# Kernel tuning notes

Measured on AMD Instinct MI355X. Metric: run time of the kernel, lower is better.

## Reference

```python
import jax, jax.numpy as jnp
import numpy as np

B, D_IN, D_HID, NH, PF = 1024, 2048, 4096, 8, 2
D_UP = D_IN * PF          # 4096
HS = D_HID // NH          # 512 head size
EPS = 1e-5


def setup_inputs() -> dict:
    key = jax.random.key(0)
    ks = jax.random.split(key, 24)
    it = iter(range(24))

    def lin(k, fin, fout):
        # weight stored as (in, out); y = x @ W + b
        return jax.random.normal(k, (fin, fout), jnp.float32) / np.float32(np.sqrt(fin))

    def bd(k, fin_blk, fout_blk):
        # block-diagonal per-head weights (NH, in_blk, out_blk)
        return jax.random.normal(k, (NH, fin_blk, fout_blk), jnp.float32) / np.float32(np.sqrt(fin_blk))

    inp = {}
    inp['x'] = jax.random.normal(ks[next(it)], (B, D_IN), jnp.float32)
    inp['h_prev'] = jax.random.normal(ks[next(it)], (B, D_HID), jnp.float32)
    inp['c_prev'] = jax.random.normal(ks[next(it)], (B, D_HID), jnp.float32)
    inp['n_prev'] = jax.random.normal(ks[next(it)], (B, D_HID), jnp.float32)
    inp['m_prev'] = jax.random.normal(ks[next(it)], (B, D_HID), jnp.float32)
    inp['ln_w'] = jnp.ones((D_IN,), jnp.float32)
    inp['ln_b'] = jnp.zeros((D_IN,), jnp.float32)
    inp['upL_w'] = lin(ks[next(it)], D_IN, D_UP); inp['upL_b'] = jnp.zeros((D_UP,), jnp.float32)
    inp['upR_w'] = lin(ks[next(it)], D_IN, D_HID); inp['upR_b'] = jnp.zeros((D_HID,), jnp.float32)
    inp['conv_w'] = jax.random.normal(ks[next(it)], (1, 1, 4), jnp.float32) * 0.5  # (O,I,K)
    inp['conv_b'] = jnp.zeros((1,), jnp.float32)
    inp['skip_w'] = lin(ks[next(it)], D_UP, D_HID); inp['skip_b'] = jnp.zeros((D_HID,), jnp.float32)
    inp['wq'] = bd(ks[next(it)], D_UP // NH, HS); inp['bq'] = jnp.zeros((NH, HS), jnp.float32)
    inp['wk'] = bd(ks[next(it)], D_UP // NH, HS); inp['bk'] = jnp.zeros((NH, HS), jnp.float32)
    inp['wv'] = bd(ks[next(it)], D_UP // NH, HS); inp['bv'] = jnp.zeros((NH, HS), jnp.float32)
    inp['wi_w'] = lin(ks[next(it)], D_UP, D_HID); inp['wi_b'] = jnp.zeros((D_HID,), jnp.float32)
    inp['wf_w'] = lin(ks[next(it)], D_UP, D_HID); inp['wf_b'] = jnp.zeros((D_HID,), jnp.float32)
    inp['wo_w'] = lin(ks[next(it)], D_UP, D_HID); inp['wo_b'] = jnp.zeros((D_HID,), jnp.float32)
    inp['gn_w'] = jnp.ones((D_HID,), jnp.float32)
    inp['gn_b'] = jnp.zeros((D_HID,), jnp.float32)
    inp['down_w'] = lin(ks[next(it)], D_HID, D_IN); inp['down_b'] = jnp.zeros((D_IN,), jnp.float32)
    return inp


def _forward(x, h_prev, c_prev, n_prev, m_prev, ln_w, ln_b, upL_w, upL_b, upR_w, upR_b,
             conv_w, conv_b, skip_w, skip_b, wq, bq, wk, bk, wv, bv,
             wi_w, wi_b, wf_w, wf_b, wo_w, wo_b, gn_w, gn_b, down_w, down_b):
    b = x.shape[0]
    # LayerNorm(input_size)
    mu = jnp.mean(x, axis=-1, keepdims=True)
    var = jnp.var(x, axis=-1, keepdims=True)
    x_norm = (x - mu) * jax.lax.rsqrt(var + EPS) * ln_w + ln_b

    x_up_left = x_norm @ upL_w + upL_b     # (B, D_UP)
    x_up_right = x_norm @ upR_w + upR_b    # (B, D_HID)

    # CausalConv1D(1,1,4): left-pad 3, valid conv  == torch pad 3 both sides + drop last 3
    conv = jax.lax.conv_general_dilated(
        x_up_left[:, None, :], conv_w, window_strides=(1,), padding=((3, 0),),
        dimension_numbers=('NCH', 'OIH', 'NCH'))
    x_conv = jax.nn.silu(conv[:, 0, :] + conv_b[0])   # (B, D_UP)

    x_skip = x_conv @ skip_w + skip_b                 # (B, D_HID)

    def blockdiag(xv, w, bias):
        xh = xv.reshape(b, NH, -1)                    # (B, NH, in_blk)
        return (jnp.einsum('bhi,hio->bho', xh, w) + bias).reshape(b, -1)

    q = blockdiag(x_conv, wq, bq)                                  # (B, D_HID)
    k = blockdiag(x_conv, wk, bk) / np.float32(np.sqrt(HS))
    v = blockdiag(x_up_left, wv, bv)

    i_tilde = x_conv @ wi_w + wi_b
    f_tilde = x_conv @ wf_w + wf_b
    o = jax.nn.sigmoid(x_up_left @ wo_w + wo_b)

    # stabilized exponential gating
    m_t = jnp.maximum(f_tilde + m_prev, i_tilde)
    i_g = jnp.exp(i_tilde - m_t)
    f_g = jnp.exp(f_tilde + m_prev - m_t)
    c_t = f_g * c_prev + i_g * (v * k)
    n_t = f_g * n_prev + i_g * k

    # torch.max(torch.abs(n_t.T @ q), 1)[0] -> (D_HID,)
    denom = jnp.max(jnp.abs(n_t.T @ q), axis=1)
    h_t = o * (c_t * q) / denom                       # broadcast (B,D_HID)/(D_HID,)

    # GroupNorm(NH, D_HID) on 2D input
    hg = h_t.reshape(b, NH, HS)
    mu_g = jnp.mean(hg, axis=-1, keepdims=True)
    var_g = jnp.var(hg, axis=-1, keepdims=True)
    gn = ((hg - mu_g) * jax.lax.rsqrt(var_g + EPS)).reshape(b, D_HID) * gn_w + gn_b

    out = (gn + x_skip) * jax.nn.silu(x_up_right)
    final = out @ down_w + down_b + x
    return final, h_t, c_t, n_t, m_t


def reference(x, h_prev, c_prev, n_prev, m_prev, ln_w, ln_b, upL_w, upL_b, upR_w, upR_b,
              conv_w, conv_b, skip_w, skip_b, wq, bq, wk, bk, wv, bv,
              wi_w, wi_b, wf_w, wf_b, wo_w, wo_b, gn_w, gn_b, down_w, down_b):
    return _forward(x, h_prev, c_prev, n_prev, m_prev, ln_w, ln_b, upL_w, upL_b, upR_w, upR_b,
                    conv_w, conv_b, skip_w, skip_b, wq, bq, wk, bk, wv, bv,
                    wi_w, wi_b, wf_w, wf_b, wo_w, wo_b, gn_w, gn_b, down_w, down_b)
```

## Files before the change

kernel.cpp:

```cpp
#include <hip/hip_runtime.h>
#include <math.h>

#define B_ROWS 1024
#define D_IN   2048
#define D_HID  4096
#define D_UP   4096
#define NH     8
#define HS     512
#define LN_EPS 1e-5f

typedef __attribute__((ext_vector_type(8))) short bf16x8_t;
typedef __attribute__((ext_vector_type(4))) float f32x4_t;
typedef __attribute__((ext_vector_type(4))) unsigned short us4_t;

__device__ __forceinline__ unsigned short f2bf(float f) {
    unsigned int u = __float_as_uint(f);
    u += 0x7fffu + ((u >> 16) & 1u);
    return (unsigned short)(u >> 16);
}
__device__ __forceinline__ float bf2f(unsigned short u) {
    return __uint_as_float(((unsigned int)u) << 16);
}
__device__ __forceinline__ float sigmoidf_(float x) { return 1.0f / (1.0f + expf(-x)); }
__device__ __forceinline__ float siluf_(float x)    { return x / (1.0f + expf(-x)); }

__device__ __forceinline__ void gload16(const unsigned short* g, unsigned short* l) {
    __builtin_amdgcn_global_load_lds(
        (const __attribute__((address_space(1))) unsigned int*)(const void*)g,
        (__attribute__((address_space(3))) unsigned int*)(void*)l,
        16, 0, 0);
}

#define VMW(n) asm volatile("s_waitcnt vmcnt(" #n ")" ::: "memory")

#define XCD_SWZ()                                                        \
    int bx = blockIdx.x, by = blockIdx.y;                                \
    {                                                                    \
        const int gx_ = gridDim.x;                                       \
        const int n_  = gx_ * gridDim.y;                                 \
        if ((n_ & 7) == 0) {                                             \
            int lin = by * gx_ + bx;                                     \
            const int q8 = n_ >> 3;                                      \
            lin = (lin & 7) * q8 + (lin >> 3);                           \
            bx = lin % gx_; by = lin / gx_;                              \
        }                                                                \
    }

struct MGChunk {
    const unsigned short* A;
    const unsigned short* Bt;
    const float* bias;
    const float* resid;
    float* C;
    unsigned short* C2;
    float* denom;
    float alpha;
    int epi;
};

template<int NCH>
__global__ __launch_bounds__(256, 3) void mg256(
    MGChunk c0, MGChunk c1, MGChunk c2, MGChunk c3,
    int K, int lda, int ldbt, int ldc, int bpc,
    long aB, long wB, long bB, long cB)
{
    const int gx = gridDim.x, gy = gridDim.y;
    const int n = gx * gy;
    const int orig = blockIdx.y * gx + blockIdx.x;
    const int wl = ((n & 7) == 0) ? ((orig & 7) * (n >> 3) + (orig >> 3)) : orig;
    const int bxw = wl / gy;
    const int byw = wl - bxw * gy;
    const int chid = (NCH > 1) ? (bxw / bpc) : 0;
    const int cbx = bxw - chid * bpc;
    const MGChunk ch = (chid == 0) ? c0 : ((chid == 1) ? c1 : ((chid == 2) ? c2 : c3));
    const int bz = blockIdx.z;

    const unsigned short* A  = ch.A  + bz * aB;
    const unsigned short* Bt = ch.Bt + bz * wB;

    __shared__ __align__(16) unsigned short As[2][256][32];
    __shared__ __align__(16) unsigned short Bs[2][128][32];

    const int t = threadIdx.x;
    const int w = t >> 6, l = t & 63;
    const int wrm = w >> 1;
    const int wcn = w & 1;
    const long rowA = (long)byw * 256;
    const long rowB = (long)cbx * 128;

    const int skz = (((l & 3) ^ ((l >> 3) & 3)) << 3);
    const unsigned short* Ag = A  + rowA * (long)lda;
    const unsigned short* Bg = Bt + rowB * (long)ldbt;

    const int lm  = l & 15;
    const int pkz = (((l >> 4) ^ ((l >> 1) & 3)) << 3);

    f32x4_t acc[8][4];
#pragma unroll
    for (int mi = 0; mi < 8; ++mi)
#pragma unroll
        for (int ni = 0; ni < 4; ++ni) acc[mi][ni] = (f32x4_t)0.0f;

#define STAGE(buf, kb)                                                        \
    {                                                                         \
        _Pragma("unroll")                                                     \
        for (int p = 0; p < 4; ++p)                                           \
            gload16(Ag + (long)(w * 64 + p * 16 + (l >> 2)) * lda + (kb) + skz, \
                    &As[buf][w * 64 + p * 16][0]);                            \
        _Pragma("unroll")                                                     \
        for (int p = 0; p < 2; ++p)                                           \
            gload16(Bg + (long)(w * 32 + p * 16 + (l >> 2)) * ldbt + (kb) + skz, \
                    &Bs[buf][w * 32 + p * 16][0]);                            \
    }

    const int nsteps = K >> 5;
    STAGE(0, 0);

    int cur = 0;
    for (int ti = 0; ti < nsteps; ++ti) {
        if (ti + 1 < nsteps) {
            STAGE(cur ^ 1, (ti + 1) << 5);
            VMW(6);
        } else {
            VMW(0);
        }
        __builtin_amdgcn_s_barrier();

        bf16x8_t bfr[4];
#pragma unroll
        for (int ni = 0; ni < 4; ++ni)
            bfr[ni] = *(const bf16x8_t*)&Bs[cur][wcn * 64 + ni * 16 + lm][pkz];
#pragma unroll
        for (int mi = 0; mi < 8; ++mi) {
            const bf16x8_t af = *(const bf16x8_t*)&As[cur][wrm * 128 + mi * 16 + lm][pkz];
#pragma unroll
            for (int ni = 0; ni < 4; ++ni)
                acc[mi][ni] = __builtin_amdgcn_mfma_f32_16x16x32_bf16(
                    af, bfr[ni], acc[mi][ni], 0, 0, 0);
        }

        asm volatile("s_waitcnt lgkmcnt(0)" ::: "memory");
        __builtin_amdgcn_s_barrier();
        cur ^= 1;
    }
#undef STAGE

    const int lr4 = (l >> 4) * 4;
    if (ch.epi == 3) {
        float rmax[8][4];
#pragma unroll
        for (int mi = 0; mi < 8; ++mi)
#pragma unroll
            for (int r = 0; r < 4; ++r) {
                float m = 0.0f;
#pragma unroll
                for (int ni = 0; ni < 4; ++ni) m = fmaxf(m, fabsf(acc[mi][ni][r]));
                rmax[mi][r] = m;
            }
#pragma unroll
        for (int off = 1; off < 16; off <<= 1)
#pragma unroll
            for (int mi = 0; mi < 8; ++mi)
#pragma unroll
                for (int r = 0; r < 4; ++r)
                    rmax[mi][r] = fmaxf(rmax[mi][r], __shfl_xor(rmax[mi][r], off, 64));
        if (lm == 0) {
#pragma unroll
            for (int mi = 0; mi < 8; ++mi)
#pragma unroll
                for (int r = 0; r < 4; ++r) {
                    const long m = rowA + wrm * 128 + mi * 16 + lr4 + r;
                    atomicMax((unsigned int*)&ch.denom[m], __float_as_uint(rmax[mi][r]));
                }
        }
        return;
    }
    const float* bias = ch.bias + bz * bB;
#pragma unroll
    for (int mi = 0; mi < 8; ++mi) {
        const long m0 = rowA + wrm * 128 + mi * 16 + lr4;
#pragma unroll
        for (int ni = 0; ni < 4; ++ni) {
            const long nn = rowB + wcn * 64 + ni * 16 + lm;
            const float bv = bias[nn];
#pragma unroll
            for (int r = 0; r < 4; ++r) {
                float v = acc[mi][ni][r] + bv;
                if (ch.epi == 2) v *= ch.alpha;
                const long m = m0 + r;
                if (ch.epi == 5) (ch.C2 + bz * cB)[m * ldc + nn] = f2bf(v);
                else             (ch.C  + bz * cB)[m * ldc + nn] = v;
            }
        }
    }
}

struct MCChunk {
    const unsigned short* A;
    const unsigned short* Bt;
    const float* bias;
    float* C;
    unsigned short* C2;
    float alpha;
    int epi;
};

template<int NCH>
__global__ __launch_bounds__(256) void mgemm_mc(
    MCChunk c0, MCChunk c1, MCChunk c2,
    int K, int lda, int ldbt, int ldc, int bpc,
    long aB, long wB, long bB, long cB)
{
    XCD_SWZ();
    const int chid = bx / bpc;
    const int cbx  = bx - chid * bpc;
    const MCChunk ch = (chid == 0) ? c0 : ((NCH > 1 && chid == 1) ? c1 : c2);
    const int bz = blockIdx.z;

    const unsigned short* A  = ch.A  + bz * aB;
    const unsigned short* Bt = ch.Bt + bz * wB;
    const float* bias = ch.bias + bz * bB;

    __shared__ __align__(16) unsigned short As[2][128][40];
    __shared__ __align__(16) unsigned short Bs[2][128][40];

    const int t = threadIdx.x;
    const int w = t >> 6, l = t & 63;
    const int wr = w >> 1, wc = w & 1;
    const long rowA = (long)by * 128;
    const long rowB = (long)cbx * 128;

    const int lr = t >> 2;
    const int lc = (t & 3) << 3;
    const unsigned short* Ag = A  + (rowA + lr) * (long)lda  + lc;
    const unsigned short* Bg = Bt + (rowB + lr) * (long)ldbt + lc;

    const int lm = l & 15;
    const int lk = (l >> 4) * 8;

    f32x4_t acc[4][4];
#pragma unroll
    for (int mi = 0; mi < 4; ++mi)
#pragma unroll
        for (int ni = 0; ni < 4; ++ni) acc[mi][ni] = (f32x4_t)0.0f;

    bf16x8_t ra[2], rb[2];
#pragma unroll
    for (int p = 0; p < 2; ++p) {
        ra[p] = *(const bf16x8_t*)(Ag + (long)p * 64 * lda);
        rb[p] = *(const bf16x8_t*)(Bg + (long)p * 64 * ldbt);
    }
#pragma unroll
    for (int p = 0; p < 2; ++p) {
        *(bf16x8_t*)&As[0][lr + p * 64][lc] = ra[p];
        *(bf16x8_t*)&Bs[0][lr + p * 64][lc] = rb[p];
    }
    __syncthreads();

    const int nsteps = K >> 5;
    for (int ti = 0; ti < nsteps; ++ti) {
        const int cur = ti & 1;
        if (ti + 1 < nsteps) {
            const int kb = (ti + 1) << 5;
#pragma unroll
            for (int p = 0; p < 2; ++p) {
                ra[p] = *(const bf16x8_t*)(Ag + (long)p * 64 * lda  + kb);
                rb[p] = *(const bf16x8_t*)(Bg + (long)p * 64 * ldbt + kb);
            }
        }
        bf16x8_t af[4], bfr[4];
#pragma unroll
        for (int mi = 0; mi < 4; ++mi)
            af[mi] = *(const bf16x8_t*)&As[cur][wr * 64 + mi * 16 + lm][lk];
#pragma unroll
        for (int ni = 0; ni < 4; ++ni)
            bfr[ni] = *(const bf16x8_t*)&Bs[cur][wc * 64 + ni * 16 + lm][lk];
#pragma unroll
        for (int mi = 0; mi < 4; ++mi)
#pragma unroll
            for (int ni = 0; ni < 4; ++ni)
                acc[mi][ni] = __builtin_amdgcn_mfma_f32_16x16x32_bf16(
                    af[mi], bfr[ni], acc[mi][ni], 0, 0, 0);
        if (ti + 1 < nsteps) {
            const int nxt = cur ^ 1;
#pragma unroll
            for (int p = 0; p < 2; ++p) {
                *(bf16x8_t*)&As[nxt][lr + p * 64][lc] = ra[p];
                *(bf16x8_t*)&Bs[nxt][lr + p * 64][lc] = rb[p];
            }
        }
        __syncthreads();
    }

    const int lr4 = (l >> 4) * 4;
    const float alpha = ch.alpha;
#pragma unroll
    for (int mi = 0; mi < 4; ++mi) {
        const long m0 = rowA + wr * 64 + mi * 16 + lr4;
#pragma unroll
        for (int ni = 0; ni < 4; ++ni) {
            const long nn = rowB + wc * 64 + ni * 16 + lm;
            const float bv = bias[nn];
#pragma unroll
            for (int r = 0; r < 4; ++r) {
                const float v = (acc[mi][ni][r] + bv) * alpha;
                const long m = m0 + r;
                if (ch.epi == 5) (ch.C2 + bz * cB)[m * ldc + nn] = f2bf(v);
                else             (ch.C  + bz * cB)[m * ldc + nn] = v;
            }
        }
    }
}

template<int BM, int EPI>
__global__ __launch_bounds__(256) void mgemm(
    const unsigned short* __restrict__ A, const unsigned short* __restrict__ Bt,
    const float* __restrict__ bias, const float* __restrict__ resid,
    float* __restrict__ C, float* __restrict__ denom,
    int K, int lda, int ldbt, int ldc)
{
    constexpr int MR = BM / 32;
    constexpr int AP = BM / 64;
    XCD_SWZ();

    __shared__ __align__(16) unsigned short As[2][BM][40];
    __shared__ __align__(16) unsigned short Bs[2][128][40];

    const int t = threadIdx.x;
    const int w = t >> 6, l = t & 63;
    const int wr = w >> 1, wc = w & 1;
    const long rowA = (long)by * BM;
    const long rowB = (long)bx * 128;

    const int lr = t >> 2;
    const int lc = (t & 3) << 3;
    const unsigned short* Ag = A  + (rowA + lr) * (long)lda  + lc;
    const unsigned short* Bg = Bt + (rowB + lr) * (long)ldbt + lc;

    const int lm = l & 15;
    const int lk = (l >> 4) * 8;

    f32x4_t acc[MR][4];
#pragma unroll
    for (int mi = 0; mi < MR; ++mi)
#pragma unroll
        for (int ni = 0; ni < 4; ++ni) acc[mi][ni] = (f32x4_t)0.0f;

    bf16x8_t ra[AP], rb[2];
#pragma unroll
    for (int p = 0; p < AP; ++p) ra[p] = *(const bf16x8_t*)(Ag + (long)p * 64 * lda);
#pragma unroll
    for (int p = 0; p < 2;  ++p) rb[p] = *(const bf16x8_t*)(Bg + (long)p * 64 * ldbt);
#pragma unroll
    for (int p = 0; p < AP; ++p) *(bf16x8_t*)&As[0][lr + p * 64][lc] = ra[p];
#pragma unroll
    for (int p = 0; p < 2;  ++p) *(bf16x8_t*)&Bs[0][lr + p * 64][lc] = rb[p];
    __syncthreads();

    const int nsteps = K >> 5;
    for (int ti = 0; ti < nsteps; ++ti) {
        const int cur = ti & 1;
        if (ti + 1 < nsteps) {
            const int kb = (ti + 1) << 5;
#pragma unroll
            for (int p = 0; p < AP; ++p) ra[p] = *(const bf16x8_t*)(Ag + (long)p * 64 * lda  + kb);
#pragma unroll
            for (int p = 0; p < 2;  ++p) rb[p] = *(const bf16x8_t*)(Bg + (long)p * 64 * ldbt + kb);
        }
        bf16x8_t af[MR], bfr[4];
#pragma unroll
        for (int mi = 0; mi < MR; ++mi)
            af[mi] = *(const bf16x8_t*)&As[cur][wr * (BM / 2) + mi * 16 + lm][lk];
#pragma unroll
        for (int ni = 0; ni < 4; ++ni)
            bfr[ni] = *(const bf16x8_t*)&Bs[cur][wc * 64 + ni * 16 + lm][lk];
#pragma unroll
        for (int mi = 0; mi < MR; ++mi)
#pragma unroll
            for (int ni = 0; ni < 4; ++ni)
                acc[mi][ni] = __builtin_amdgcn_mfma_f32_16x16x32_bf16(
                    af[mi], bfr[ni], acc[mi][ni], 0, 0, 0);
        if (ti + 1 < nsteps) {
            const int nxt = cur ^ 1;
#pragma unroll
            for (int p = 0; p < AP; ++p) *(bf16x8_t*)&As[nxt][lr + p * 64][lc] = ra[p];
#pragma unroll
            for (int p = 0; p < 2;  ++p) *(bf16x8_t*)&Bs[nxt][lr + p * 64][lc] = rb[p];
        }
        __syncthreads();
    }

    const int lr4 = (l >> 4) * 4;
#pragma unroll
    for (int mi = 0; mi < MR; ++mi) {
        const long m0 = rowA + wr * (BM / 2) + mi * 16 + lr4;
#pragma unroll
        for (int ni = 0; ni < 4; ++ni) {
            const long nn = rowB + wc * 64 + ni * 16 + lm;
            const float bv = bias[nn];
#pragma unroll
            for (int r = 0; r < 4; ++r) {
                float v = acc[mi][ni][r] + bv;
                const long m = m0 + r;
                if (EPI == 4) v += resid[m * ldc + nn];
                C[m * ldc + nn] = v;
            }
        }
    }
}

struct TP4 {
    const float* s0; const float* s1; const float* s2; const float* s3;
    unsigned short* d0; unsigned short* d1; unsigned short* d2; unsigned short* d3;
};

__global__ __launch_bounds__(256) void tp_batch(TP4 tp, int R, int C)
{
    const int z = blockIdx.z;
    const float* X = (z == 0) ? tp.s0 : (z == 1) ? tp.s1 : (z == 2) ? tp.s2 : tp.s3;
    unsigned short* XT = (z == 0) ? tp.d0 : (z == 1) ? tp.d1 : (z == 2) ? tp.d2 : tp.d3;
    __shared__ float tile[64][65];
    const int t = threadIdx.x;
    const long r0 = (long)blockIdx.y * 64;
    const long c0 = (long)blockIdx.x * 64;
    const int tr = t >> 4;
    const int tc = (t & 15) << 2;
#pragma unroll
    for (int p = 0; p < 4; ++p) {
        const float4 v = *(const float4*)(X + (r0 + tr + p * 16) * C + c0 + tc);
        tile[tr + p * 16][tc + 0] = v.x;
        tile[tr + p * 16][tc + 1] = v.y;
        tile[tr + p * 16][tc + 2] = v.z;
        tile[tr + p * 16][tc + 3] = v.w;
    }
    __syncthreads();
#pragma unroll
    for (int p = 0; p < 2; ++p) {
        const int orow = (t >> 3) + p * 32;
        const int oc8  = (t & 7) * 8;
        unsigned short tmp[8];
#pragma unroll
        for (int j = 0; j < 8; ++j) tmp[j] = f2bf(tile[oc8 + j][orow]);
        *(bf16x8_t*)(XT + (c0 + orow) * (long)R + r0 + oc8) = *(const bf16x8_t*)tmp;
    }
}

__global__ __launch_bounds__(256) void tp_qkv(
    const float* wq, const float* wk, const float* wv, unsigned short* dst)
{
    const int z = blockIdx.z;
    const int sel = z >> 3, head = z & 7;
    const float* X = ((sel == 0) ? wq : (sel == 1) ? wk : wv) + (long)head * HS * HS;
    unsigned short* XT = dst + (long)sel * NH * HS * HS + (long)head * HS * HS;
    __shared__ float tile[64][65];
    const int t = threadIdx.x;
    const long r0 = (long)blockIdx.y * 64;
    const long c0 = (long)blockIdx.x * 64;
    const int tr = t >> 4;
    const int tc = (t & 15) << 2;
#pragma unroll
    for (int p = 0; p < 4; ++p) {
        const float4 v = *(const float4*)(X + (r0 + tr + p * 16) * HS + c0 + tc);
        tile[tr + p * 16][tc + 0] = v.x;
        tile[tr + p * 16][tc + 1] = v.y;
        tile[tr + p * 16][tc + 2] = v.z;
        tile[tr + p * 16][tc + 3] = v.w;
    }
    __syncthreads();
#pragma unroll
    for (int p = 0; p < 2; ++p) {
        const int orow = (t >> 3) + p * 32;
        const int oc8  = (t & 7) * 8;
        unsigned short tmp[8];
#pragma unroll
        for (int j = 0; j < 8; ++j) tmp[j] = f2bf(tile[oc8 + j][orow]);
        *(bf16x8_t*)(XT + (c0 + orow) * (long)HS + r0 + oc8) = *(const bf16x8_t*)tmp;
    }
}

__global__ __launch_bounds__(256) void layernorm_kernel(
    const float* __restrict__ x, const float* __restrict__ w,
    const float* __restrict__ b, unsigned short* __restrict__ out)
{
    __shared__ float sh[8];
    const int row = blockIdx.x, t = threadIdx.x;
    const float* xr = x + (long)row * D_IN;
    float v[8];
    float s = 0.f, ss = 0.f;
#pragma unroll
    for (int i = 0; i < 8; ++i) {
        v[i] = xr[t + 256 * i];
        s += v[i];
        ss += v[i] * v[i];
    }
#pragma unroll
    for (int off = 32; off; off >>= 1) {
        s  += __shfl_down(s, off, 64);
        ss += __shfl_down(ss, off, 64);
    }
    const int lane = t & 63, wid = t >> 6;
    if (lane == 0) { sh[wid * 2] = s; sh[wid * 2 + 1] = ss; }
    __syncthreads();
    s = 0.f; ss = 0.f;
#pragma unroll
    for (int i = 0; i < 4; ++i) { s += sh[i * 2]; ss += sh[i * 2 + 1]; }
    const float mu  = s * (1.0f / D_IN);
    const float var = ss * (1.0f / D_IN) - mu * mu;
    const float rs  = rsqrtf(var + LN_EPS);
    unsigned short* orow = out + (long)row * D_IN;
#pragma unroll
    for (int i = 0; i < 8; ++i) {
        const int d = t + 256 * i;
        orow[d] = f2bf((v[i] - mu) * rs * w[d] + b[d]);
    }
}

__global__ void conv_silu_kernel(const unsigned short* __restrict__ xl,
                                 const float* __restrict__ cw,
                                 const float* __restrict__ cb,
                                 unsigned short* __restrict__ out)
{
    const long idx = (long)blockIdx.x * blockDim.x + threadIdx.x;
    if (idx >= (long)B_ROWS * D_UP) return;
    const int d = (int)(idx & (D_UP - 1));
    const float w0 = cw[0], w1 = cw[1], w2 = cw[2], w3 = cw[3];
    float acc = cb[0] + w3 * bf2f(xl[idx]);
    if (d >= 1) acc += w2 * bf2f(xl[idx - 1]);
    if (d >= 2) acc += w1 * bf2f(xl[idx - 2]);
    if (d >= 3) acc += w0 * bf2f(xl[idx - 3]);
    out[idx] = f2bf(siluf_(acc));
}

__global__ void gating_kernel(const float4* __restrict__ it, const float4* __restrict__ ft,
                              const float4* __restrict__ mp, const float4* __restrict__ cp,
                              const float4* __restrict__ np_, const float4* __restrict__ kk,
                              const float4* __restrict__ vv,
                              float4* __restrict__ mt, float4* __restrict__ ct,
                              float4* __restrict__ nt)
{
    const long idx = (long)blockIdx.x * blockDim.x + threadIdx.x;
    if (idx >= (long)B_ROWS * D_HID / 4) return;
    const float4 i4 = it[idx], f4 = ft[idx], mp4 = mp[idx];
    const float4 cp4 = cp[idx], np4 = np_[idx], k4 = kk[idx], v4 = vv[idx];
    float4 m4, c4, n4;
#pragma unroll
    for (int j = 0; j < 4; ++j) {
        const float i_t = (&i4.x)[j];
        const float f_t = (&f4.x)[j] + (&mp4.x)[j];
        const float m_t = fmaxf(f_t, i_t);
        const float i_g = expf(i_t - m_t);
        const float f_g = expf(f_t - m_t);
        const float kv  = (&k4.x)[j];
        (&c4.x)[j] = f_g * (&cp4.x)[j] + i_g * ((&v4.x)[j] * kv);
        (&n4.x)[j] = f_g * (&np4.x)[j] + i_g * kv;
        (&m4.x)[j] = m_t;
    }
    ct[idx] = c4;
    nt[idx] = n4;
    mt[idx] = m4;
}

__global__ __launch_bounds__(128) void hgnorm_kernel(
    const unsigned short* __restrict__ op, const float* __restrict__ ct,
    const float* __restrict__ qb, const float* __restrict__ denom,
    const float* __restrict__ gw, const float* __restrict__ gb,
    const unsigned short* __restrict__ xskip, const unsigned short* __restrict__ xupR,
    float* __restrict__ ht, unsigned short* __restrict__ out)
{
    __shared__ float sh[4];
    const int b = blockIdx.x >> 3, h = blockIdx.x & 7;
    const int t = threadIdx.x;
    const long base = (long)b * D_HID + h * HS;
    float v[4];
    float s = 0.f, ss = 0.f;
#pragma unroll
    for (int i = 0; i < 4; ++i) {
        const long ix = base + t + 128 * i;
        const int  dg = h * HS + t + 128 * i;
        const float hv = sigmoidf_(bf2f(op[ix])) * ct[ix] * qb[ix] / denom[dg];
        ht[ix] = hv;
        v[i] = hv;
        s += hv;
        ss += hv * hv;
    }
#pragma unroll
    for (int off = 32; off; off >>= 1) {
        s  += __shfl_down(s, off, 64);
        ss += __shfl_down(ss, off, 64);
    }
    if ((t & 63) == 0) { sh[(t >> 6) * 2] = s; sh[(t >> 6) * 2 + 1] = ss; }
    __syncthreads();
    s = sh[0] + sh[2];
    ss = sh[1] + sh[3];
    const float mu  = s * (1.0f / HS);
    const float var = ss * (1.0f / HS) - mu * mu;
    const float rs  = rsqrtf(var + LN_EPS);
#pragma unroll
    for (int i = 0; i < 4; ++i) {
        const int  dg = h * HS + t + 128 * i;
        const long ix = base + t + 128 * i;
        const float g = (v[i] - mu) * rs * gw[dg] + gb[dg];
        out[ix] = f2bf((g + bf2f(xskip[ix])) * siluf_(bf2f(xupR[ix])));
    }
}

extern "C" void kernel_launch(void* const* d_in, const int* in_sizes, int n_in,
                              void* d_out, int out_size, void* d_ws, size_t ws_size,
                              hipStream_t stream)
{
    const float* x      = (const float*)d_in[0];
    const float* c_prev = (const float*)d_in[2];
    const float* n_prev = (const float*)d_in[3];
    const float* m_prev = (const float*)d_in[4];
    const float* ln_w   = (const float*)d_in[5];
    const float* ln_b   = (const float*)d_in[6];
    const float* upL_w  = (const float*)d_in[7];
    const float* upL_b  = (const float*)d_in[8];
    const float* upR_w  = (const float*)d_in[9];
    const float* upR_b  = (const float*)d_in[10];
    const float* conv_w = (const float*)d_in[11];
    const float* conv_b = (const float*)d_in[12];
    const float* skip_w = (const float*)d_in[13];
    const float* skip_b = (const float*)d_in[14];
    const float* wq     = (const float*)d_in[15];
    const float* bq     = (const float*)d_in[16];
    const float* wk     = (const float*)d_in[17];
    const float* bk     = (const float*)d_in[18];
    const float* wv     = (const float*)d_in[19];
    const float* bv     = (const float*)d_in[20];
    const float* wi_w   = (const float*)d_in[21];
    const float* wi_b   = (const float*)d_in[22];
    const float* wf_w   = (const float*)d_in[23];
    const float* wf_b   = (const float*)d_in[24];
    const float* wo_w   = (const float*)d_in[25];
    const float* wo_b   = (const float*)d_in[26];
    const float* gn_w   = (const float*)d_in[27];
    const float* gn_b   = (const float*)d_in[28];
    const float* down_w = (const float*)d_in[29];
    const float* down_b = (const float*)d_in[30];

    float* out     = (float*)d_out;
    float* final_o = out;
    float* ht      = final_o + 2097152;
    float* ct      = ht + 4194304;
    float* nt      = ct + 4194304;
    float* mt      = nt + 4194304;

    unsigned short* WTA = (unsigned short*)ht;
    unsigned short* WTB = (unsigned short*)nt;

    const long M = 1048576;
    float* ws = (float*)d_ws;
    float* qb  = ws +  0 * M;
    float* kb  = ws +  4 * M;
    float* vb  = ws +  8 * M;
    float* itb = ws + 12 * M;
    float* ftb = ws + 16 * M;
    unsigned short* xupR_bf  = (unsigned short*)(ws + 20 * M);
    unsigned short* xskip_bf = (unsigned short*)(ws + 22 * M);
    unsigned short* opb_bf   = (unsigned short*)(ws + 24 * M);
    unsigned short* xnorm_bf = (unsigned short*)(ws + 26 * M);
    unsigned short* xupL_bf  = (unsigned short*)(ws + 27 * M);
    unsigned short* xconv_bf = (unsigned short*)(ws + 29 * M);
    float* denom             = ws + 31 * M;
    unsigned short* WTC      = (unsigned short*)(ws + 32 * M);
    unsigned short* WTD      = (unsigned short*)(ws +  0 * M);
    unsigned short* ntT      = (unsigned short*)(ws + 26 * M);
    unsigned short* qT       = (unsigned short*)(ws + 28 * M);
    unsigned short* dwT      = (unsigned short*)(ws + 12 * M);
    unsigned short* tmp_bf   = (unsigned short*)(ws +  8 * M);

    const float kscale = 1.0f / sqrtf((float)HS);
    const long HS2 = (long)HS * HS;
    MGChunk cz = {};
    MCChunk mz = {};

    layernorm_kernel<<<B_ROWS, 256, 0, stream>>>(x, ln_w, ln_b, xnorm_bf);

    {
        TP4 tp = { upL_w, upR_w, nullptr, nullptr, WTA, WTA + 8388608, nullptr, nullptr };
        tp_batch<<<dim3(64, 32, 2), 256, 0, stream>>>(tp, D_IN, D_UP);
    }
    {
        MCChunk a = { xnorm_bf, WTA,           upL_b, nullptr, xupL_bf, 1.0f, 5 };
        MCChunk b = { xnorm_bf, WTA + 8388608, upR_b, nullptr, xupR_bf, 1.0f, 5 };
        mgemm_mc<2><<<dim3(64, 8, 1), 256, 0, stream>>>(
            a, b, mz, D_IN, D_IN, D_IN, D_HID, 32, 0, 0, 0, 0);
    }

    conv_silu_kernel<<<(B_ROWS * D_UP) / 256, 256, 0, stream>>>(xupL_bf, conv_w, conv_b, xconv_bf);

    {
        TP4 tp = { skip_w, wi_w, wf_w, wo_w, WTA, WTB, WTC, WTD };
        tp_batch<<<dim3(64, 64, 4), 256, 0, stream>>>(tp, D_UP, D_HID);
    }
    {
        MGChunk a = { xconv_bf, WTA, skip_b, nullptr, nullptr, xskip_bf, nullptr, 1.0f, 5 };
        MGChunk b = { xconv_bf, WTB, wi_b,   nullptr, itb,     nullptr,  nullptr, 1.0f, 0 };
        MGChunk c = { xconv_bf, WTC, wf_b,   nullptr, ftb,     nullptr,  nullptr, 1.0f, 0 };
        MGChunk d = { xupL_bf,  WTD, wo_b,   nullptr, nullptr, opb_bf,   nullptr, 1.0f, 5 };
        mg256<4><<<dim3(128, 4, 1), 256, 0, stream>>>(
            a, b, c, d, D_UP, D_UP, D_UP, D_HID, 32, 0, 0, 0, 0);
    }

    tp_qkv<<<dim3(8, 8, 24), 256, 0, stream>>>(wq, wk, wv, WTA);
    {
        MCChunk a = { xconv_bf, WTA,                bq, qb, nullptr, 1.0f,   0 };
        MCChunk b = { xconv_bf, WTA + NH * HS2,     bk, kb, nullptr, kscale, 0 };
        MCChunk c = { xupL_bf,  WTA + 2 * NH * HS2, bv, vb, nullptr, 1.0f,   0 };
        mgemm_mc<3><<<dim3(12, 8, NH), 256, 0, stream>>>(
            a, b, c, HS, D_UP, HS, D_HID, 4, HS, HS2, HS, HS);
    }

    gating_kernel<<<(B_ROWS * D_HID / 4) / 256, 256, 0, stream>>>(
        (const float4*)itb, (const float4*)ftb, (const float4*)m_prev,
        (const float4*)c_prev, (const float4*)n_prev, (const float4*)kb,
        (const float4*)vb, (float4*)mt, (float4*)ct, (float4*)nt);

    {
        TP4 tp = { nt, qb, nullptr, nullptr, ntT, qT, nullptr, nullptr };
        tp_batch<<<dim3(64, 16, 2), 256, 0, stream>>>(tp, B_ROWS, D_HID);
    }
    hipMemsetAsync(denom, 0, D_HID * sizeof(float), stream);
    {
        MGChunk a = { ntT, qT, nullptr, nullptr, nullptr, nullptr, denom, 1.0f, 3 };
        mg256<1><<<dim3(32, 16, 1), 256, 0, stream>>>(
            a, cz, cz, cz, B_ROWS, B_ROWS, B_ROWS, 0, 32, 0, 0, 0, 0);
    }

    {
        TP4 tp = { down_w, nullptr, nullptr, nullptr, dwT, nullptr, nullptr, nullptr };
        tp_batch<<<dim3(32, 64, 1), 256, 0, stream>>>(tp, D_HID, D_IN);
    }

    hgnorm_kernel<<<B_ROWS * NH, 128, 0, stream>>>(
        opb_bf, ct, qb, denom, gn_w, gn_b, xskip_bf, xupR_bf, ht, tmp_bf);

    mgemm<64, 4><<<dim3(16, 16, 1), 256, 0, stream>>>(
        tmp_bf, dwT, down_b, x, final_o, nullptr, D_HID, D_HID, D_HID, D_IN);
}
```

Measured before the change: 555.9 us.

## Merge big gate GEMMs and per-head QKV GEMMs into one launch

Replaces the separate 4-chunk skip/i/f/o GEMM launch and the per-head QKV GEMM launch with a single kernel. Block ids are remapped with an XCD swizzle and dispatched to either a K=4096 gate tile or a K=512 head tile, so the small QKV work fills leftover slots in the wave of large tiles and one launch is saved. K and V are now written as bf16 instead of fp32, which halves their write and read traffic in the gating kernel at the cost of some precision. Blocks do unequal amounts of work, so load imbalance across the grid is possible.

After: 656.5 us. 18.1% more time.

```diff
diff --git a/kernel.cpp b/kernel.cpp
--- a/kernel.cpp
+++ b/kernel.cpp
@@ -46,6 +46,144 @@
         }                                                                \
     }
 
+__global__ __launch_bounds__(256, 3) void mg_mega(
+    const unsigned short* __restrict__ xconv, const unsigned short* __restrict__ xupL,
+    const unsigned short* __restrict__ sT, const unsigned short* __restrict__ iT,
+    const unsigned short* __restrict__ fT, const unsigned short* __restrict__ oT,
+    const unsigned short* __restrict__ qkvT,
+    const float* __restrict__ skip_b, const float* __restrict__ wi_b,
+    const float* __restrict__ wf_b, const float* __restrict__ wo_b,
+    const float* __restrict__ bq, const float* __restrict__ bk,
+    const float* __restrict__ bv,
+    unsigned short* __restrict__ xskip, float* __restrict__ itb,
+    float* __restrict__ ftb, unsigned short* __restrict__ opb,
+    float* __restrict__ qb, unsigned short* __restrict__ kb_bf,
+    unsigned short* __restrict__ vb_bf, float kscale)
+{
+    const int gy = gridDim.y;
+    const int n = gridDim.x * gy;
+    const int orig = blockIdx.y * gridDim.x + blockIdx.x;
+    const int wl = (orig & 7) * (n >> 3) + (orig >> 3);
+    const int bxw = wl / gy;
+    const int byw = wl - bxw * gy;
+
+    const unsigned short *Ap, *Btp;
+    const float* biasp;
+    float* Cp = nullptr;
+    unsigned short* C2p = nullptr;
+    int Kloc, ldbt, rowBl;
+    float alpha = 1.0f;
+    bool bf16out;
+    if (bxw < 128) {
+        const int chid = bxw >> 5;
+        rowBl = (bxw & 31) * 128;
+        Kloc = 4096; ldbt = 4096;
+        Ap = (chid == 3) ? xupL : xconv;
+        Btp = (chid == 0) ? sT : (chid == 1) ? iT : (chid == 2) ? fT : oT;
+        biasp = (chid == 0) ? skip_b : (chid == 1) ? wi_b : (chid == 2) ? wf_b : wo_b;
+        bf16out = (chid == 0) || (chid == 3);
+        C2p = (chid == 0) ? xskip : opb;
+        Cp  = (chid == 1) ? itb : ftb;
+    } else {
+        const int j = bxw - 128;
+        const int mat = j >> 2;
+        rowBl = (j & 3) * 128;
+        const int sel = mat >> 3, head = mat & 7;
+        Kloc = 512; ldbt = 512;
+        Ap = ((sel == 2) ? xupL : xconv) + head * 512;
+        Btp = qkvT + (long)mat * (HS * HS);
+        biasp = ((sel == 0) ? bq : (sel == 1) ? bk : bv) + head * 512;
+        alpha = (sel == 1) ? kscale : 1.0f;
+        bf16out = (sel != 0);
+        Cp  = qb + head * 512;
+        C2p = ((sel == 1) ? kb_bf : vb_bf) + head * 512;
+    }
+
+    __shared__ __align__(16) unsigned short As[2][256][32];
+    __shared__ __align__(16) unsigned short Bs[2][128][32];
+
+    const int t = threadIdx.x;
+    const int w = t >> 6, l = t & 63;
+    const int wrm = w >> 1;
+    const int wcn = w & 1;
+    const long rowA = (long)byw * 256;
+
+    const int skz = (((l & 3) ^ ((l >> 3) & 3)) << 3);
+    const unsigned short* Ag = Ap  + rowA * 4096L;
+    const unsigned short* Bg = Btp + (long)rowBl * ldbt;
+
+    const int lm  = l & 15;
+    const int pkz = (((l >> 4) ^ ((l >> 1) & 3)) << 3);
+
+    f32x4_t acc[8][4];
+#pragma unroll
+    for (int mi = 0; mi < 8; ++mi)
+#pragma unroll
+        for (int ni = 0; ni < 4; ++ni) acc[mi][ni] = (f32x4_t)0.0f;
+
+#define STAGE(buf, kb)                                                        \
+    {                                                                         \
+        _Pragma("unroll")                                                     \
+        for (int p = 0; p < 4; ++p)                                           \
+            gload16(Ag + (long)(w * 64 + p * 16 + (l >> 2)) * 4096 + (kb) + skz, \
+                    &As[buf][w * 64 + p * 16][0]);                            \
+        _Pragma("unroll")                                                     \
+        for (int p = 0; p < 2; ++p)                                           \
+            gload16(Bg + (long)(w * 32 + p * 16 + (l >> 2)) * ldbt + (kb) + skz, \
+                    &Bs[buf][w * 32 + p * 16][0]);                            \
+    }
+
+    const int nsteps = Kloc >> 5;
+    STAGE(0, 0);
+
+    int cur = 0;
+    for (int ti = 0; ti < nsteps; ++ti) {
+        if (ti + 1 < nsteps) {
+            STAGE(cur ^ 1, (ti + 1) << 5);
+            VMW(6);
+        } else {
+            VMW(0);
+        }
+        __builtin_amdgcn_s_barrier();
+
+        bf16x8_t bfr[4];
+#pragma unroll
+        for (int ni = 0; ni < 4; ++ni)
+            bfr[ni] = *(const bf16x8_t*)&Bs[cur][wcn * 64 + ni * 16 + lm][pkz];
+#pragma unroll
+        for (int mi = 0; mi < 8; ++mi) {
+            const bf16x8_t af = *(const bf16x8_t*)&As[cur][wrm * 128 + mi * 16 + lm][pkz];
+#pragma unroll
+            for (int ni = 0; ni < 4; ++ni)
+                acc[mi][ni] = __builtin_amdgcn_mfma_f32_16x16x32_bf16(
+                    af, bfr[ni], acc[mi][ni], 0, 0, 0);
+        }
+
+        asm volatile("s_waitcnt lgkmcnt(0)" ::: "memory");
+        __builtin_amdgcn_s_barrier();
+        cur ^= 1;
+    }
+#undef STAGE
+
+    const int lr4 = (l >> 4) * 4;
+#pragma unroll
+    for (int mi = 0; mi < 8; ++mi) {
+        const long m0 = rowA + wrm * 128 + mi * 16 + lr4;
+#pragma unroll
+        for (int ni = 0; ni < 4; ++ni) {
+            const int nn = rowBl + wcn * 64 + ni * 16 + lm;
+            const float bv4 = biasp[nn];
+#pragma unroll
+            for (int r = 0; r < 4; ++r) {
+                const float v = (acc[mi][ni][r] + bv4) * alpha;
+                const long m = m0 + r;
+                if (bf16out) C2p[m * 4096 + nn] = f2bf(v);
+                else         Cp [m * 4096 + nn] = v;
+            }
+        }
+    }
+}
+
 struct MGChunk {
     const unsigned short* A;
     const unsigned short* Bt;
@@ -533,15 +671,16 @@
 
 __global__ void gating_kernel(const float4* __restrict__ it, const float4* __restrict__ ft,
                               const float4* __restrict__ mp, const float4* __restrict__ cp,
-                              const float4* __restrict__ np_, const float4* __restrict__ kk,
-                              const float4* __restrict__ vv,
+                              const float4* __restrict__ np_, const us4_t* __restrict__ kk,
+                              const us4_t* __restrict__ vv,
                               float4* __restrict__ mt, float4* __restrict__ ct,
                               float4* __restrict__ nt)
 {
     const long idx = (long)blockIdx.x * blockDim.x + threadIdx.x;
     if (idx >= (long)B_ROWS * D_HID / 4) return;
     const float4 i4 = it[idx], f4 = ft[idx], mp4 = mp[idx];
-    const float4 cp4 = cp[idx], np4 = np_[idx], k4 = kk[idx], v4 = vv[idx];
+    const float4 cp4 = cp[idx], np4 = np_[idx];
+    const us4_t k4 = kk[idx], v4 = vv[idx];
     float4 m4, c4, n4;
 #pragma unroll
     for (int j = 0; j < 4; ++j) {
@@ -550,8 +689,8 @@
         const float m_t = fmaxf(f_t, i_t);
         const float i_g = expf(i_t - m_t);
         const float f_g = expf(f_t - m_t);
-        const float kv  = (&k4.x)[j];
-        (&c4.x)[j] = f_g * (&cp4.x)[j] + i_g * ((&v4.x)[j] * kv);
+        const float kv  = bf2f(k4[j]);
+        (&c4.x)[j] = f_g * (&cp4.x)[j] + i_g * (bf2f(v4[j]) * kv);
         (&n4.x)[j] = f_g * (&np4.x)[j] + i_g * kv;
         (&m4.x)[j] = m_t;
     }
@@ -651,9 +790,9 @@
 
     const long M = 1048576;
     float* ws = (float*)d_ws;
-    float* qb  = ws +  0 * M;
-    float* kb  = ws +  4 * M;
-    float* vb  = ws +  8 * M;
+    unsigned short* WTD      = (unsigned short*)(ws +  0 * M);
+    unsigned short* kb_bf    = (unsigned short*)(ws +  8 * M);
+    unsigned short* vb_bf    = (unsigned short*)(ws + 10 * M);
     float* itb = ws + 12 * M;
     float* ftb = ws + 16 * M;
     unsigned short* xupR_bf  = (unsigned short*)(ws + 20 * M);
@@ -664,14 +803,14 @@
     unsigned short* xconv_bf = (unsigned short*)(ws + 29 * M);
     float* denom             = ws + 31 * M;
     unsigned short* WTC      = (unsigned short*)(ws + 32 * M);
-    unsigned short* WTD      = (unsigned short*)(ws +  0 * M);
+    unsigned short* qkvT     = (unsigned short*)(ws + 40 * M);
+    float* qb                = ws + 43 * M;
     unsigned short* ntT      = (unsigned short*)(ws + 26 * M);
     unsigned short* qT       = (unsigned short*)(ws + 28 * M);
     unsigned short* dwT      = (unsigned short*)(ws + 12 * M);
     unsigned short* tmp_bf   = (unsigned short*)(ws +  8 * M);
 
     const float kscale = 1.0f / sqrtf((float)HS);
-    const long HS2 = (long)HS * HS;
     MGChunk cz = {};
     MCChunk mz = {};
 
@@ -694,28 +833,17 @@
         TP4 tp = { skip_w, wi_w, wf_w, wo_w, WTA, WTB, WTC, WTD };
         tp_batch<<<dim3(64, 64, 4), 256, 0, stream>>>(tp, D_UP, D_HID);
     }
-    {
-        MGChunk a = { xconv_bf, WTA, skip_b, nullptr, nullptr, xskip_bf, nullptr, 1.0f, 5 };
-        MGChunk b = { xconv_bf, WTB, wi_b,   nullptr, itb,     nullptr,  nullptr, 1.0f, 0 };
-        MGChunk c = { xconv_bf, WTC, wf_b,   nullptr, ftb,     nullptr,  nullptr, 1.0f, 0 };
-        MGChunk d = { xupL_bf,  WTD, wo_b,   nullptr, nullptr, opb_bf,   nullptr, 1.0f, 5 };
-        mg256<4><<<dim3(128, 4, 1), 256, 0, stream>>>(
-            a, b, c, d, D_UP, D_UP, D_UP, D_HID, 32, 0, 0, 0, 0);
-    }
-
-    tp_qkv<<<dim3(8, 8, 24), 256, 0, stream>>>(wq, wk, wv, WTA);
-    {
-        MCChunk a = { xconv_bf, WTA,                bq, qb, nullptr, 1.0f,   0 };
-        MCChunk b = { xconv_bf, WTA + NH * HS2,     bk, kb, nullptr, kscale, 0 };
-        MCChunk c = { xupL_bf,  WTA + 2 * NH * HS2, bv, vb, nullptr, 1.0f,   0 };
-        mgemm_mc<3><<<dim3(12, 8, NH), 256, 0, stream>>>(
-            a, b, c, HS, D_UP, HS, D_HID, 4, HS, HS2, HS, HS);
-    }
+    tp_qkv<<<dim3(8, 8, 24), 256, 0, stream>>>(wq, wk, wv, qkvT);
+
+    mg_mega<<<dim3(224, 4, 1), 256, 0, stream>>>(
+        xconv_bf, xupL_bf, WTA, WTB, WTC, WTD, qkvT,
+        skip_b, wi_b, wf_b, wo_b, bq, bk, bv,
+        xskip_bf, itb, ftb, opb_bf, qb, kb_bf, vb_bf, kscale);
 
     gating_kernel<<<(B_ROWS * D_HID / 4) / 256, 256, 0, stream>>>(
         (const float4*)itb, (const float4*)ftb, (const float4*)m_prev,
-        (const float4*)c_prev, (const float4*)n_prev, (const float4*)kb,
-        (const float4*)vb, (float4*)mt, (float4*)ct, (float4*)nt);
+        (const float4*)c_prev, (const float4*)n_prev, (const us4_t*)kb_bf,
+        (const us4_t*)vb_bf, (float4*)mt, (float4*)ct, (float4*)nt);
 
     {
         TP4 tp = { nt, qb, nullptr, nullptr, ntT, qT, nullptr, nullptr };
```
